# Kernel optimization log

Measured on AMD Instinct MI355X. Metric: run time of the kernel, lower is better.

## Reference

```python
import jax, jax.numpy as jnp
import numpy as np

D_MODEL = 1024
PATTERNS = 8
BETA = 1.0


def setup_inputs() -> dict:
    key = jax.random.key(0)
    k_h, k_p, k_w, k_b = jax.random.split(key, 4)
    h = jax.random.normal(k_h, (8, 8192, D_MODEL), dtype=jnp.float32)
    patterns = jax.random.normal(k_p, (PATTERNS, D_MODEL), dtype=jnp.float32)
    # nn.Linear(d_model, d_model): weight [out, in], bias [out]
    bound = 1.0 / np.sqrt(D_MODEL)
    proj_w = jax.random.uniform(k_w, (D_MODEL, D_MODEL), minval=-bound, maxval=bound, dtype=jnp.float32)
    proj_b = jax.random.uniform(k_b, (D_MODEL,), minval=-bound, maxval=bound, dtype=jnp.float32)
    return {"h": h, "patterns": patterns, "proj_w": proj_w, "proj_b": proj_b}


def reference(h, patterns, proj_w, proj_b):
    # scores: [B, S, P] = softmax(beta * h @ patterns^T)
    scores = jax.nn.softmax(BETA * jnp.einsum("bsd,pd->bsp", h, patterns), axis=-1)
    # read: [B, S, D]
    read = jnp.einsum("bsp,pd->bsd", scores, patterns)
    # proj(h + read): Linear applies x @ W^T + b
    return jnp.einsum("bsd,ed->bse", h + read, proj_w) + proj_b
```

## Files before the change

kernel.cpp:

```cpp
#include <hip/hip_runtime.h>
#include <hip/hip_bf16.h>
#include <stdint.h>

#define DM 1024
#define NPAT 8
#define NKT 16
#define LDS_A 0
#define LDS_B 65536

typedef __bf16 bf16x8_t __attribute__((ext_vector_type(8)));
typedef float f32x4_t __attribute__((ext_vector_type(4)));
typedef unsigned short u16;

typedef const __attribute__((address_space(1))) void* gas_ptr;
typedef __attribute__((address_space(3))) void* las_ptr;

__device__ __forceinline__ u16 f2bf(float x) {
  uint32_t u = __float_as_uint(x);
  uint32_t r = (u + 0x7FFFu + ((u >> 16) & 1u)) >> 16;
  return (u16)r;
}

__global__ __launch_bounds__(256) void k0_cvt_w(const float* __restrict__ w,
                                                u16* __restrict__ wb) {
  int i = blockIdx.x * 256 + threadIdx.x;
  float4 v = ((const float4*)w)[i];
  ushort4 o;
  o.x = f2bf(v.x); o.y = f2bf(v.y); o.z = f2bf(v.z); o.w = f2bf(v.w);
  ((ushort4*)wb)[i] = o;
}

__global__ __launch_bounds__(256) void k1_hopfield(const float* __restrict__ h,
                                                   const float* __restrict__ pat,
                                                   u16* __restrict__ A, int M) {
  __shared__ float patL[NPAT * DM];
  const int tid = threadIdx.x;
  {
    const float4* p4 = (const float4*)pat;
    float4* l4 = (float4*)patL;
#pragma unroll
    for (int i = 0; i < (NPAT * DM / 4) / 256; ++i)
      l4[i * 256 + tid] = p4[i * 256 + tid];
  }
  __syncthreads();

  const int lane = tid & 63;
  const int wid = (blockIdx.x << 2) | (tid >> 6);
  const int nw = gridDim.x << 2;
  const float4* h4 = (const float4*)h;
  const float4* pl4 = (const float4*)patL;
  ushort4* A4 = (ushort4*)A;

  for (int rp = wid; rp < (M >> 1); rp += nw) {
    const size_t r0 = (size_t)rp << 1;
    float4 hv0[4], hv1[4];
#pragma unroll
    for (int j = 0; j < 4; ++j) {
      hv0[j] = h4[r0 * 256 + j * 64 + lane];
      hv1[j] = h4[(r0 + 1) * 256 + j * 64 + lane];
    }
    float d0[NPAT], d1[NPAT];
#pragma unroll
    for (int p = 0; p < NPAT; ++p) {
      float a = 0.f, b = 0.f;
#pragma unroll
      for (int j = 0; j < 4; ++j) {
        float4 pv = pl4[p * 256 + j * 64 + lane];
        a = fmaf(hv0[j].x, pv.x, a); a = fmaf(hv0[j].y, pv.y, a);
        a = fmaf(hv0[j].z, pv.z, a); a = fmaf(hv0[j].w, pv.w, a);
        b = fmaf(hv1[j].x, pv.x, b); b = fmaf(hv1[j].y, pv.y, b);
        b = fmaf(hv1[j].z, pv.z, b); b = fmaf(hv1[j].w, pv.w, b);
      }
      d0[p] = a; d1[p] = b;
    }
#pragma unroll
    for (int p = 0; p < NPAT; ++p) {
#pragma unroll
      for (int o = 32; o > 0; o >>= 1) {
        d0[p] += __shfl_xor(d0[p], o);
        d1[p] += __shfl_xor(d1[p], o);
      }
    }
    float m0 = d0[0], m1 = d1[0];
#pragma unroll
    for (int p = 1; p < NPAT; ++p) { m0 = fmaxf(m0, d0[p]); m1 = fmaxf(m1, d1[p]); }
    float s0 = 0.f, s1 = 0.f;
#pragma unroll
    for (int p = 0; p < NPAT; ++p) {
      d0[p] = __expf(d0[p] - m0); s0 += d0[p];
      d1[p] = __expf(d1[p] - m1); s1 += d1[p];
    }
    const float i0 = 1.f / s0, i1 = 1.f / s1;
#pragma unroll
    for (int p = 0; p < NPAT; ++p) { d0[p] *= i0; d1[p] *= i1; }

#pragma unroll
    for (int j = 0; j < 4; ++j) {
      float4 a0 = hv0[j], a1 = hv1[j];
#pragma unroll
      for (int p = 0; p < NPAT; ++p) {
        float4 pv = pl4[p * 256 + j * 64 + lane];
        a0.x = fmaf(d0[p], pv.x, a0.x); a0.y = fmaf(d0[p], pv.y, a0.y);
        a0.z = fmaf(d0[p], pv.z, a0.z); a0.w = fmaf(d0[p], pv.w, a0.w);
        a1.x = fmaf(d1[p], pv.x, a1.x); a1.y = fmaf(d1[p], pv.y, a1.y);
        a1.z = fmaf(d1[p], pv.z, a1.z); a1.w = fmaf(d1[p], pv.w, a1.w);
      }
      ushort4 o0, o1;
      o0.x = f2bf(a0.x); o0.y = f2bf(a0.y); o0.z = f2bf(a0.z); o0.w = f2bf(a0.w);
      o1.x = f2bf(a1.x); o1.y = f2bf(a1.y); o1.z = f2bf(a1.z); o1.w = f2bf(a1.w);
      A4[r0 * 256 + j * 64 + lane] = o0;
      A4[(r0 + 1) * 256 + j * 64 + lane] = o1;
    }
  }
}

#define STAGE(matBase, regionOff, kt, hf, bufOff)                                        \
  do {                                                                                   \
    const u16* _s = (matBase) + (size_t)((hf)*128) * DM + (kt)*64;                       \
    char* _d = lds + (regionOff) + (bufOff) + (hf)*16384;                                \
    __builtin_amdgcn_global_load_lds((gas_ptr)(_s + go0), (las_ptr)(_d + L0), 16, 0, 0); \
    __builtin_amdgcn_global_load_lds((gas_ptr)(_s + go1), (las_ptr)(_d + L1), 16, 0, 0); \
  } while (0)

#define RD(p) (*(const bf16x8_t*)(p))

__global__ __launch_bounds__(512, 2) void k2_gemm(const u16* __restrict__ A,
                                                  const u16* __restrict__ B,
                                                  const float* __restrict__ bias,
                                                  float* __restrict__ C, int M) {
  __shared__ __align__(16) char lds[131072];
  const int tid = threadIdx.x;
  const int lane = tid & 63;
  const int wave = tid >> 6;
  const int wm = wave >> 2;
  const int wn = wave & 3;
  const int r16 = lane & 15, kg = lane >> 4;

  const int bid = blockIdx.x;
  const int swz = (bid & 7) * 128 + (bid >> 3);
  const int tn = swz & 3, tm = swz >> 2;

  const u16* Ab = A + (size_t)tm * 256 * DM;
  const u16* Bb = B + (size_t)tn * 256 * DM;

  const uint32_t L0 = (uint32_t)tid * 16;
  const uint32_t L1 = 8192u + (uint32_t)tid * 16;
  const uint32_t S0 = L0 ^ (((L0 >> 7) & 7u) << 4);
  const uint32_t S1 = L1 ^ (((L1 >> 7) & 7u) << 4);
  const uint32_t go0 = (S0 >> 7) * DM + ((S0 & 127u) >> 1);
  const uint32_t go1 = (S1 >> 7) * DM + ((S1 & 127u) >> 1);

  const uint32_t flip = (uint32_t)(r16 & 7) << 4;
  const uint32_t aoff0 = ((uint32_t)(r16 * 128 + kg * 16)) ^ flip;
  const uint32_t aoff1 = ((uint32_t)(r16 * 128 + 64 + kg * 16)) ^ flip;
  const uint32_t brow = (uint32_t)((wn & 1) * 64 + r16);
  const uint32_t boff0 = ((uint32_t)(brow * 128 + kg * 16)) ^ flip;
  const uint32_t boff1 = ((uint32_t)(brow * 128 + 64 + kg * 16)) ^ flip;
  const uint32_t aHalfSel = (uint32_t)wm * 16384;
  const uint32_t bHalfSel = (uint32_t)(wn >> 1) * 16384;

  f32x4_t acc[8][4] = {};
  bf16x8_t aq[4][2], bl[2][2], bh[2][2];

  STAGE(Bb, LDS_B, 0, 0, 0);
  STAGE(Ab, LDS_A, 0, 0, 0);
  STAGE(Bb, LDS_B, 0, 1, 0);
  STAGE(Ab, LDS_A, 0, 1, 0);
  STAGE(Bb, LDS_B, 1, 0, 32768);
  STAGE(Ab, LDS_A, 1, 0, 32768);
  asm volatile("s_waitcnt vmcnt(4)");
  __builtin_amdgcn_s_barrier();

  for (int t = 0; t < NKT; ++t) {
    const uint32_t co = (uint32_t)(t & 1) << 15;
    const uint32_t no = co ^ 32768u;
    const char* a0 = lds + LDS_A + co + aHalfSel + aoff0;
    const char* a1 = lds + LDS_A + co + aHalfSel + aoff1;
    const char* b0 = lds + LDS_B + co + bHalfSel + boff0;
    const char* b1 = lds + LDS_B + co + bHalfSel + boff1;

#pragma unroll
    for (int m = 0; m < 4; ++m) { aq[m][0] = RD(a0 + m * 2048); aq[m][1] = RD(a1 + m * 2048); }
#pragma unroll
    for (int n = 0; n < 2; ++n) { bl[n][0] = RD(b0 + n * 2048); bl[n][1] = RD(b1 + n * 2048); }
    if (t + 1 < NKT) STAGE(Bb, LDS_B, t + 1, 1, no);
    __builtin_amdgcn_s_barrier();
    asm volatile("s_waitcnt lgkmcnt(0)");
    __builtin_amdgcn_s_setprio(1);
#pragma unroll
    for (int m = 0; m < 4; ++m)
#pragma unroll
      for (int n = 0; n < 2; ++n)
#pragma unroll
        for (int ks = 0; ks < 2; ++ks)
          acc[m][n] = __builtin_amdgcn_mfma_f32_16x16x32_bf16(aq[m][ks], bl[n][ks], acc[m][n], 0, 0, 0);
    __builtin_amdgcn_s_setprio(0);
    __builtin_amdgcn_s_barrier();

#pragma unroll
    for (int n = 0; n < 2; ++n) { bh[n][0] = RD(b0 + (n + 2) * 2048); bh[n][1] = RD(b1 + (n + 2) * 2048); }
    if (t + 1 < NKT) STAGE(Ab, LDS_A, t + 1, 1, no);
    __builtin_amdgcn_s_barrier();
    asm volatile("s_waitcnt lgkmcnt(0)");
    __builtin_amdgcn_s_setprio(1);
#pragma unroll
    for (int m = 0; m < 4; ++m)
#pragma unroll
      for (int n = 0; n < 2; ++n)
#pragma unroll
        for (int ks = 0; ks < 2; ++ks)
          acc[m][n + 2] = __builtin_amdgcn_mfma_f32_16x16x32_bf16(aq[m][ks], bh[n][ks], acc[m][n + 2], 0, 0, 0);
    __builtin_amdgcn_s_setprio(0);
    __builtin_amdgcn_s_barrier();

#pragma unroll
    for (int m = 0; m < 4; ++m) { aq[m][0] = RD(a0 + (m + 4) * 2048); aq[m][1] = RD(a1 + (m + 4) * 2048); }
    if (t + 2 < NKT) STAGE(Bb, LDS_B, t + 2, 0, co);
    __builtin_amdgcn_s_barrier();
    asm volatile("s_waitcnt lgkmcnt(0)");
    __builtin_amdgcn_s_setprio(1);
#pragma unroll
    for (int m = 0; m < 4; ++m)
#pragma unroll
      for (int n = 0; n < 2; ++n)
#pragma unroll
        for (int ks = 0; ks < 2; ++ks)
          acc[m + 4][n] = __builtin_amdgcn_mfma_f32_16x16x32_bf16(aq[m][ks], bl[n][ks], acc[m + 4][n], 0, 0, 0);
    __builtin_amdgcn_s_setprio(0);
    __builtin_amdgcn_s_barrier();

    if (t + 2 < NKT) STAGE(Ab, LDS_A, t + 2, 0, co);
    __builtin_amdgcn_s_barrier();
    __builtin_amdgcn_s_setprio(1);
#pragma unroll
    for (int m = 0; m < 4; ++m)
#pragma unroll
      for (int n = 0; n < 2; ++n)
#pragma unroll
        for (int ks = 0; ks < 2; ++ks)
          acc[m + 4][n + 2] = __builtin_amdgcn_mfma_f32_16x16x32_bf16(aq[m][ks], bh[n][ks], acc[m + 4][n + 2], 0, 0, 0);
    __builtin_amdgcn_s_setprio(0);
    if (t < NKT - 1) {
      if (t + 2 < NKT) asm volatile("s_waitcnt vmcnt(4)");
      else             asm volatile("s_waitcnt vmcnt(0)");
    }
    __builtin_amdgcn_s_barrier();
  }

  const int colB = tn * 256 + wn * 64 + r16;
  const int rowB = tm * 256 + wm * 128 + kg * 4;
  float bvv[4];
#pragma unroll
  for (int n = 0; n < 4; ++n) bvv[n] = bias[colB + n * 16];
#pragma unroll
  for (int m = 0; m < 8; ++m) {
#pragma unroll
    for (int r = 0; r < 4; ++r) {
      float* cp = C + (size_t)(rowB + m * 16 + r) * DM + colB;
#pragma unroll
      for (int n = 0; n < 4; ++n) cp[n * 16] = acc[m][n][r] + bvv[n];
    }
  }
}

extern "C" void kernel_launch(void* const* d_in, const int* in_sizes, int n_in,
                              void* d_out, int out_size, void* d_ws, size_t ws_size,
                              hipStream_t stream) {
  const float* h = (const float*)d_in[0];
  const float* pat = (const float*)d_in[1];
  const float* w = (const float*)d_in[2];
  const float* b = (const float*)d_in[3];
  float* out = (float*)d_out;
  const int M = in_sizes[0] / DM;

  u16* Wb = (u16*)d_ws;
  u16* Abf = (u16*)d_ws + (size_t)DM * DM;

  k0_cvt_w<<<DM * DM / 4 / 256, 256, 0, stream>>>(w, Wb);
  k1_hopfield<<<2048, 256, 0, stream>>>(h, pat, Abf, M);
  k2_gemm<<<(M / 256) * (DM / 256), 512, 0, stream>>>(Abf, Wb, b, out, M);
}
```

Measured before the change: 252.3 us.

## Make each GEMM block sweep all four N tiles in one continuous pipeline

```diff
diff --git a/kernel.cpp b/kernel.cpp
--- a/kernel.cpp
+++ b/kernel.cpp
@@ -4,7 +4,6 @@
 
 #define DM 1024
 #define NPAT 8
-#define NKT 16
 #define LDS_A 0
 #define LDS_B 65536
 
@@ -114,9 +113,9 @@
   }
 }
 
-#define STAGE(matBase, regionOff, kt, hf, bufOff)                                        \
+#define STAGE(basePtr, regionOff, kt, hf, bufOff)                                        \
   do {                                                                                   \
-    const u16* _s = (matBase) + (size_t)((hf)*128) * DM + (kt)*64;                       \
+    const u16* _s = (basePtr) + (size_t)((hf)*128) * DM + (kt)*64;                       \
     char* _d = lds + (regionOff) + (bufOff) + (hf)*16384;                                \
     __builtin_amdgcn_global_load_lds((gas_ptr)(_s + go0), (las_ptr)(_d + L0), 16, 0, 0); \
     __builtin_amdgcn_global_load_lds((gas_ptr)(_s + go1), (las_ptr)(_d + L1), 16, 0, 0); \
@@ -136,12 +135,8 @@
   const int wn = wave & 3;
   const int r16 = lane & 15, kg = lane >> 4;
 
-  const int bid = blockIdx.x;
-  const int swz = (bid & 7) * 128 + (bid >> 3);
-  const int tn = swz & 3, tm = swz >> 2;
-
+  const int tm = blockIdx.x;
   const u16* Ab = A + (size_t)tm * 256 * DM;
-  const u16* Bb = B + (size_t)tn * 256 * DM;
 
   const uint32_t L0 = (uint32_t)tid * 16;
   const uint32_t L1 = 8192u + (uint32_t)tid * 16;
@@ -159,20 +154,23 @@
   const uint32_t aHalfSel = (uint32_t)wm * 16384;
   const uint32_t bHalfSel = (uint32_t)(wn >> 1) * 16384;
 
+  const int rowB = tm * 256 + wm * 128 + kg * 4;
+
   f32x4_t acc[8][4] = {};
   bf16x8_t aq[4][2], bl[2][2], bh[2][2];
 
-  STAGE(Bb, LDS_B, 0, 0, 0);
+  STAGE(B, LDS_B, 0, 0, 0);
   STAGE(Ab, LDS_A, 0, 0, 0);
-  STAGE(Bb, LDS_B, 0, 1, 0);
+  STAGE(B, LDS_B, 0, 1, 0);
   STAGE(Ab, LDS_A, 0, 1, 0);
-  STAGE(Bb, LDS_B, 1, 0, 32768);
+  STAGE(B, LDS_B, 1, 0, 32768);
   STAGE(Ab, LDS_A, 1, 0, 32768);
   asm volatile("s_waitcnt vmcnt(4)");
   __builtin_amdgcn_s_barrier();
 
-  for (int t = 0; t < NKT; ++t) {
-    const uint32_t co = (uint32_t)(t & 1) << 15;
+#pragma unroll 2
+  for (int u = 0; u < 64; ++u) {
+    const uint32_t co = (uint32_t)(u & 1) << 15;
     const uint32_t no = co ^ 32768u;
     const char* a0 = lds + LDS_A + co + aHalfSel + aoff0;
     const char* a1 = lds + LDS_A + co + aHalfSel + aoff1;
@@ -183,7 +181,7 @@
     for (int m = 0; m < 4; ++m) { aq[m][0] = RD(a0 + m * 2048); aq[m][1] = RD(a1 + m * 2048); }
 #pragma unroll
     for (int n = 0; n < 2; ++n) { bl[n][0] = RD(b0 + n * 2048); bl[n][1] = RD(b1 + n * 2048); }
-    if (t + 1 < NKT) STAGE(Bb, LDS_B, t + 1, 1, no);
+    if (u + 1 < 64) STAGE(B + (size_t)((u + 1) >> 4) * 256 * DM, LDS_B, (u + 1) & 15, 1, no);
     __builtin_amdgcn_s_barrier();
     asm volatile("s_waitcnt lgkmcnt(0)");
     __builtin_amdgcn_s_setprio(1);
@@ -199,7 +197,7 @@
 
 #pragma unroll
     for (int n = 0; n < 2; ++n) { bh[n][0] = RD(b0 + (n + 2) * 2048); bh[n][1] = RD(b1 + (n + 2) * 2048); }
-    if (t + 1 < NKT) STAGE(Ab, LDS_A, t + 1, 1, no);
+    if (u + 1 < 64) STAGE(Ab, LDS_A, (u + 1) & 15, 1, no);
     __builtin_amdgcn_s_barrier();
     asm volatile("s_waitcnt lgkmcnt(0)");
     __builtin_amdgcn_s_setprio(1);
@@ -215,7 +213,7 @@
 
 #pragma unroll
     for (int m = 0; m < 4; ++m) { aq[m][0] = RD(a0 + (m + 4) * 2048); aq[m][1] = RD(a1 + (m + 4) * 2048); }
-    if (t + 2 < NKT) STAGE(Bb, LDS_B, t + 2, 0, co);
+    if (u + 2 < 64) STAGE(B + (size_t)((u + 2) >> 4) * 256 * DM, LDS_B, (u + 2) & 15, 0, co);
     __builtin_amdgcn_s_barrier();
     asm volatile("s_waitcnt lgkmcnt(0)");
     __builtin_amdgcn_s_setprio(1);
@@ -229,7 +227,7 @@
     __builtin_amdgcn_s_setprio(0);
     __builtin_amdgcn_s_barrier();
 
-    if (t + 2 < NKT) STAGE(Ab, LDS_A, t + 2, 0, co);
+    if (u + 2 < 64) STAGE(Ab, LDS_A, (u + 2) & 15, 0, co);
     __builtin_amdgcn_s_barrier();
     __builtin_amdgcn_s_setprio(1);
 #pragma unroll
@@ -240,25 +238,31 @@
         for (int ks = 0; ks < 2; ++ks)
           acc[m + 4][n + 2] = __builtin_amdgcn_mfma_f32_16x16x32_bf16(aq[m][ks], bh[n][ks], acc[m + 4][n + 2], 0, 0, 0);
     __builtin_amdgcn_s_setprio(0);
-    if (t < NKT - 1) {
-      if (t + 2 < NKT) asm volatile("s_waitcnt vmcnt(4)");
-      else             asm volatile("s_waitcnt vmcnt(0)");
-    }
-    __builtin_amdgcn_s_barrier();
-  }
-
-  const int colB = tn * 256 + wn * 64 + r16;
-  const int rowB = tm * 256 + wm * 128 + kg * 4;
-  float bvv[4];
-#pragma unroll
-  for (int n = 0; n < 4; ++n) bvv[n] = bias[colB + n * 16];
-#pragma unroll
-  for (int m = 0; m < 8; ++m) {
-#pragma unroll
-    for (int r = 0; r < 4; ++r) {
-      float* cp = C + (size_t)(rowB + m * 16 + r) * DM + colB;
-#pragma unroll
-      for (int n = 0; n < 4; ++n) cp[n * 16] = acc[m][n][r] + bvv[n];
+    if (u <= 61)      asm volatile("s_waitcnt vmcnt(4)");
+    else if (u == 62) asm volatile("s_waitcnt vmcnt(0)");
+    __builtin_amdgcn_s_barrier();
+
+    if ((u & 15) == 15) {
+      const int g = u >> 4;
+      const int colB = g * 256 + wn * 64 + r16;
+      float bvv[4];
+#pragma unroll
+      for (int n = 0; n < 4; ++n) bvv[n] = bias[colB + n * 16];
+#pragma unroll
+      for (int m = 0; m < 8; ++m) {
+#pragma unroll
+        for (int r = 0; r < 4; ++r) {
+          float* cp = C + (size_t)(rowB + m * 16 + r) * DM + colB;
+#pragma unroll
+          for (int n = 0; n < 4; ++n) cp[n * 16] = acc[m][n][r] + bvv[n];
+        }
+      }
+#pragma unroll
+      for (int m = 0; m < 8; ++m)
+#pragma unroll
+        for (int n = 0; n < 4; ++n)
+#pragma unroll
+          for (int r = 0; r < 4; ++r) acc[m][n][r] = 0.f;
     }
   }
 }
@@ -278,5 +282,5 @@
 
   k0_cvt_w<<<DM * DM / 4 / 256, 256, 0, stream>>>(w, Wb);
   k1_hopfield<<<2048, 256, 0, stream>>>(h, pat, Abf, M);
-  k2_gemm<<<(M / 256) * (DM / 256), 512, 0, stream>>>(Abf, Wb, b, out, M);
-}
+  k2_gemm<<<M / 256, 512, 0, stream>>>(Abf, Wb, b, out, M);
+}
```

After: 269.5 us. 6.8% more time.
